# Performance work log

Measured on AMD Instinct MI355X. Metric: run time of the kernel, lower is better.

The kernel has to match this reference:

```python
import jax, jax.numpy as jnp
import numpy as np

ALPHA = 1.0
MIN_FEATURE_SIZE = 1.0
SC = 1e-12
EPS_V_FLOOR = 1e-32 ** (1.0 / 6.0)  # ~4.64e-6, floor on gradient magnitude


def setup_inputs() -> dict:
    key = jax.random.key(0)
    eps = jax.random.normal(key, (8192, 8192), dtype=jnp.float32)
    grid_size = jnp.asarray(0.05, dtype=jnp.float32)
    return {"eps": eps, "grid_size": grid_size}


def _ls_derivatives(phi, d):
    # torch.gradient == numpy.gradient with edge_order=1 (central interior, one-sided edges)
    phi_x, phi_y = jnp.gradient(phi, d, d)
    phi_x = phi_x + SC
    phi_y = phi_y + SC
    phi_xx, phi_xy = jnp.gradient(phi_x, d, d)        # second derivs of phi_x
    phi_yy = jnp.gradient(phi_y, d, axis=1)           # only d/dy of phi_y is used
    return phi_x, phi_y, phi_xx, phi_xy, phi_yy


def reference(eps, grid_size):
    ex, ey, exx, exy, eyy = _ls_derivatives(eps, grid_size)
    pi_d = jnp.pi / (1.1 * MIN_FEATURE_SIZE)
    eps_v = jnp.maximum(jnp.sqrt(ex * ex + ey * ey), jnp.float32(EPS_V_FLOOR))
    k = (ex * ex * eyy - 2.0 * ex * ey * exy + ey * ey * exx) / (eps_v ** 3)
    curve_const = jnp.abs(k * jnp.arctan(eps_v / (eps + 1e-6))) - pi_d
    return jnp.nansum(ALPHA * jnp.maximum(curve_const, 0.0) * grid_size ** 2)
```

## Files before the change

kernel.cpp:

```cpp
#include <hip/hip_runtime.h>
#include <math.h>


typedef float f2 __attribute__((ext_vector_type(2)));
typedef float f4 __attribute__((ext_vector_type(4), aligned(4)));

constexpr float SCF = 1e-12f;
constexpr float EVF = 4.6415888336e-6f;
constexpr float PID = 2.8559933214452666f;
constexpr float PIH = 1.5707963268f;
constexpr int   RS  = 64;

struct Row { f4 lo, hi; };

__device__ __forceinline__ float C(const Row& r, int k) {
    return k < 4 ? r.lo[k] : r.hi[k - 4];
}
__device__ __forceinline__ void load_row(Row& r, const float* p) {
    r.lo = *(const f4*)p;
    r.hi = *(const f4*)(p + 4);
}
__device__ __forceinline__ f2 mk(float a, float b) { f2 v; v.x = a; v.y = b; return v; }
__device__ __forceinline__ f2 fma2(f2 a, f2 b, f2 c) { return __builtin_elementwise_fma(a, b, c); }
__device__ __forceinline__ f2 max2(f2 a, f2 b) { return __builtin_elementwise_max(a, b); }
__device__ __forceinline__ f2 min2(f2 a, f2 b) { return __builtin_elementwise_min(a, b); }
__device__ __forceinline__ f2 abs2(f2 a) { return __builtin_elementwise_abs(a); }
__device__ __forceinline__ f2 rcp2(f2 a) {
    return mk(__builtin_amdgcn_rcpf(a.x), __builtin_amdgcn_rcpf(a.y));
}
__device__ __forceinline__ f2 sqrt2(f2 a) {
    return mk(__builtin_amdgcn_sqrtf(a.x), __builtin_amdgcn_sqrtf(a.y));
}

__device__ __forceinline__ f2 compute_pair(const Row& R0, const Row& R1,
                                           const Row& R2, const Row& R3,
                                           const Row& R4, const Row& R5,
                                           f2 inv2d, f2 inv4dd) {
    f2 dif[6];
    #pragma unroll
    for (int k = 0; k < 6; ++k)
        dif[k] = mk(C(R3, k + 1) - C(R1, k + 1),
                    C(R4, k + 1) - C(R2, k + 1));
    f2 Pz[8];
    #pragma unroll
    for (int k = 0; k < 8; ++k)
        Pz[k] = mk(C(R2, k), C(R3, k));

    const f2 sc2 = mk(SCF, SCF);
    f2 part = mk(0.0f, 0.0f);
    #pragma unroll
    for (int q = 0; q < 4; ++q) {
        const f2 c00 = Pz[q + 2];
        const f2 ex  = fma2(dif[q + 1], inv2d, sc2);
        const f2 ey  = fma2(Pz[q + 3] - Pz[q + 1], inv2d, sc2);
        const f2 sxx = mk(C(R4, q + 2) + C(R0, q + 2),
                          C(R5, q + 2) + C(R1, q + 2));
        const f2 exx = (sxx - 2.0f * c00) * inv4dd;
        const f2 eyy = (Pz[q + 4] + Pz[q] - 2.0f * c00) * inv4dd;
        const f2 exy = (dif[q + 2] - dif[q]) * inv4dd;

        const f2 ev  = max2(sqrt2(fma2(ex, ex, ey * ey)), mk(EVF, EVF));
        const f2 num = fma2(ex * ex, eyy,
                       fma2(-2.0f * (ex * ey), exy, (ey * ey) * exx));
        const f2 kabs = abs2(num) * rcp2(ev * ev * ev);

        const f2 aw = abs2(c00 + 1e-6f);
        const f2 mx = max2(ev, aw);
        const f2 mn = min2(ev, aw);
        const f2 t  = mn * rcp2(mx);
        const f2 t2 = t * t;
        f2 pl = fma2(t2, mk(-0.01172120f, -0.01172120f), mk(0.05265332f, 0.05265332f));
        pl = fma2(t2, pl, mk(-0.11643287f, -0.11643287f));
        pl = fma2(t2, pl, mk(0.19354346f, 0.19354346f));
        pl = fma2(t2, pl, mk(-0.33262347f, -0.33262347f));
        pl = fma2(t2, pl, mk(0.99997726f, 0.99997726f));
        pl = pl * t;
        f2 at;
        at.x = (ev.x > aw.x) ? PIH - pl.x : pl.x;
        at.y = (ev.y > aw.y) ? PIH - pl.y : pl.y;

        part = part + max2(fma2(kabs, at, mk(-PID, -PID)), mk(0.0f, 0.0f));
    }
    return part;
}

__device__ __forceinline__ float eg(const float* __restrict__ e, int n, int i, int j) {
    return e[(size_t)i * (size_t)n + j];
}
__device__ __forceinline__ float gex(const float* __restrict__ e, int n, int i, int j,
                                     float inv_d, float inv_2d) {
    float v;
    if (i == 0)          v = (eg(e, n, 1, j) - eg(e, n, 0, j)) * inv_d;
    else if (i == n - 1) v = (eg(e, n, n - 1, j) - eg(e, n, n - 2, j)) * inv_d;
    else                 v = (eg(e, n, i + 1, j) - eg(e, n, i - 1, j)) * inv_2d;
    return v + SCF;
}
__device__ __forceinline__ float gey(const float* __restrict__ e, int n, int i, int j,
                                     float inv_d, float inv_2d) {
    float v;
    if (j == 0)          v = (eg(e, n, i, 1) - eg(e, n, i, 0)) * inv_d;
    else if (j == n - 1) v = (eg(e, n, i, n - 1) - eg(e, n, i, n - 2)) * inv_d;
    else                 v = (eg(e, n, i, j + 1) - eg(e, n, i, j - 1)) * inv_2d;
    return v + SCF;
}

__global__ __launch_bounds__(256, 4)
void fab_fused(const float* __restrict__ eps, const float* __restrict__ gs,
               float* __restrict__ out, int n, int G, int nfr) {
    const float d       = *gs;
    const float inv_2d  = 0.5f / d;
    const float inv_4dd = inv_2d * inv_2d;

    float acc = 0.0f;

    if (threadIdx.x < 96) {
        const int bflat = blockIdx.y * gridDim.x + blockIdx.x;
        const int idx = bflat * 96 + (int)threadIdx.x;
        if (idx < nfr) {
            const float inv_d = inv_2d + inv_2d;
            int i, j;
            if (idx < 4 * n) {
                const int rr = (idx >= n) + (idx >= 2 * n) + (idx >= 3 * n);
                j = idx - rr * n;
                i = (rr < 2) ? rr : (n - 4) + rr;
            } else {
                const int t = idx - 4 * n;
                i = 2 + (t >> 3);
                const int cc = t & 7;
                j = (cc < 4) ? cc : (n - 8) + cc;
            }

            const float ex0 = gex(eps, n, i, j, inv_d, inv_2d);
            const float ey0 = gey(eps, n, i, j, inv_d, inv_2d);

            float exx, exy, eyy;
            if (i == 0)
                exx = (gex(eps, n, 1, j, inv_d, inv_2d) - ex0) * inv_d;
            else if (i == n - 1)
                exx = (ex0 - gex(eps, n, n - 2, j, inv_d, inv_2d)) * inv_d;
            else
                exx = (gex(eps, n, i + 1, j, inv_d, inv_2d)
                     - gex(eps, n, i - 1, j, inv_d, inv_2d)) * inv_2d;

            if (j == 0)
                exy = (gex(eps, n, i, 1, inv_d, inv_2d) - ex0) * inv_d;
            else if (j == n - 1)
                exy = (ex0 - gex(eps, n, i, n - 2, inv_d, inv_2d)) * inv_d;
            else
                exy = (gex(eps, n, i, j + 1, inv_d, inv_2d)
                     - gex(eps, n, i, j - 1, inv_d, inv_2d)) * inv_2d;

            if (j == 0)
                eyy = (gey(eps, n, i, 1, inv_d, inv_2d) - ey0) * inv_d;
            else if (j == n - 1)
                eyy = (ey0 - gey(eps, n, i, n - 2, inv_d, inv_2d)) * inv_d;
            else
                eyy = (gey(eps, n, i, j + 1, inv_d, inv_2d)
                     - gey(eps, n, i, j - 1, inv_d, inv_2d)) * inv_2d;

            const float ev = fmaxf(__builtin_amdgcn_sqrtf(fmaf(ex0, ex0, ey0 * ey0)), EVF);
            const float num = fmaf(ex0 * ex0, eyy,
                              fmaf(-2.0f * ex0 * ey0, exy, ey0 * ey0 * exx));
            const float kabs = fabsf(num) * __builtin_amdgcn_rcpf(ev * ev * ev);

            const float aw = fabsf(eg(eps, n, i, j) + 1e-6f);
            const float mx = fmaxf(ev, aw);
            const float mn = fminf(ev, aw);
            const float t  = mn * __builtin_amdgcn_rcpf(mx);
            const float t2 = t * t;
            float pl = fmaf(t2, -0.01172120f, 0.05265332f);
            pl = fmaf(t2, pl, -0.11643287f);
            pl = fmaf(t2, pl, 0.19354346f);
            pl = fmaf(t2, pl, -0.33262347f);
            pl = fmaf(t2, pl, 0.99997726f);
            pl *= t;
            const float at = (ev > aw) ? (PIH - pl) : pl;

            acc += fmaxf(fmaf(kabs, at, -PID), 0.0f);
        }
    }

    {
        const int gg = blockIdx.x * 256 + threadIdx.x;
        const bool valid = (gg >= 1) && (gg <= G);
        const int gc = min(max(gg, 1), G);
        const int j  = 4 * gc;
        const int i0 = 2 + RS * blockIdx.y;
        const int count = min(RS, (n - 2) - i0);
        const float*  pj = eps + (j - 2);
        const size_t  sn = (size_t)n;
        const f2 inv2d2  = mk(inv_2d, inv_2d);
        const f2 inv4dd2 = mk(inv_4dd, inv_4dd);

        Row s0, s1, s2, s3, s4, s5, s6, s7;
        load_row(s0, pj + (size_t)(i0 - 2) * sn);
        load_row(s1, pj + (size_t)(i0 - 1) * sn);
        load_row(s2, pj + (size_t)(i0    ) * sn);
        load_row(s3, pj + (size_t)(i0 + 1) * sn);
        load_row(s4, pj + (size_t)(i0 + 2) * sn);
        load_row(s5, pj + (size_t)(i0 + 3) * sn);
        const float* pnext = pj + (size_t)(i0 + 4) * sn;

        f2 acc2 = mk(0.0f, 0.0f);
        #define PHASEP(ph, A0, A1, A2, A3, A4, A5, L0, L1)                    \
        {                                                                     \
            const int k = kbase + 2 * (ph);                                   \
            if (k < count) {                                                  \
                if (k + 2 < count) {                                          \
                    load_row(L0, pnext);                                      \
                    load_row(L1, pnext + sn);                                 \
                }                                                             \
                pnext += 2 * sn;                                              \
                acc2 = acc2 + compute_pair(A0, A1, A2, A3, A4, A5,            \
                                           inv2d2, inv4dd2);                  \
            }                                                                 \
        }

        #pragma unroll 1
        for (int kbase = 0; kbase < RS; kbase += 8) {
            PHASEP(0, s0, s1, s2, s3, s4, s5, s6, s7)
            PHASEP(1, s2, s3, s4, s5, s6, s7, s0, s1)
            PHASEP(2, s4, s5, s6, s7, s0, s1, s2, s3)
            PHASEP(3, s6, s7, s0, s1, s2, s3, s4, s5)
        }
        #undef PHASEP

        if (valid) acc += acc2.x + acc2.y;
    }

    __shared__ float wsum[4];
    #pragma unroll
    for (int off = 32; off; off >>= 1)
        acc += __shfl_down(acc, off, 64);
    if ((threadIdx.x & 63) == 0) wsum[threadIdx.x >> 6] = acc;
    __syncthreads();
    if (threadIdx.x == 0)
        atomicAdd(out, (wsum[0] + wsum[1] + wsum[2] + wsum[3]) * d * d);
}

extern "C" void kernel_launch(void* const* d_in, const int* in_sizes, int n_in,
                              void* d_out, int out_size, void* d_ws, size_t ws_size,
                              hipStream_t stream) {
    const float* eps = (const float*)d_in[0];
    const float* gs  = (const float*)d_in[1];
    float* out = (float*)d_out;

    const long long tot = (long long)in_sizes[0];
    const int n = (int)(sqrt((double)tot) + 0.5);

    hipMemsetAsync(out, 0, sizeof(float), stream);

    const int G = (n - 8) / 4;
    const int nstrip = (n - 4 + RS - 1) / RS;
    const int nfr = 4 * n + 8 * (n - 4);

    dim3 block(256, 1);
    dim3 grid(n / 1024, nstrip);
    fab_fused<<<grid, block, 0, stream>>>(eps, gs, out, n, G, nfr);
}
```

Baseline: 92.13 us.

## Align stencil column windows for 16-byte loads, use rsqrt, slot-spread atomics

```diff
diff --git a/kernel.cpp b/kernel.cpp
--- a/kernel.cpp
+++ b/kernel.cpp
@@ -3,7 +3,7 @@
 
 
 typedef float f2 __attribute__((ext_vector_type(2)));
-typedef float f4 __attribute__((ext_vector_type(4), aligned(4)));
+typedef float f4 __attribute__((ext_vector_type(4)));
 
 constexpr float SCF = 1e-12f;
 constexpr float EVF = 4.6415888336e-6f;
@@ -28,8 +28,8 @@
 __device__ __forceinline__ f2 rcp2(f2 a) {
     return mk(__builtin_amdgcn_rcpf(a.x), __builtin_amdgcn_rcpf(a.y));
 }
-__device__ __forceinline__ f2 sqrt2(f2 a) {
-    return mk(__builtin_amdgcn_sqrtf(a.x), __builtin_amdgcn_sqrtf(a.y));
+__device__ __forceinline__ f2 rsq2(f2 a) {
+    return mk(__builtin_amdgcn_rsqf(a.x), __builtin_amdgcn_rsqf(a.y));
 }
 
 __device__ __forceinline__ f2 compute_pair(const Row& R0, const Row& R1,
@@ -59,10 +59,13 @@
         const f2 eyy = (Pz[q + 4] + Pz[q] - 2.0f * c00) * inv4dd;
         const f2 exy = (dif[q + 2] - dif[q]) * inv4dd;
 
-        const f2 ev  = max2(sqrt2(fma2(ex, ex, ey * ey)), mk(EVF, EVF));
+        const f2 s2  = fma2(ex, ex, ey * ey);
+        const f2 rsq = rsq2(s2);
+        const f2 ev  = max2(s2 * rsq, mk(EVF, EVF));
+        const f2 iv3 = min2(rsq * rsq * rsq, mk(1e16f, 1e16f));
         const f2 num = fma2(ex * ex, eyy,
                        fma2(-2.0f * (ex * ey), exy, (ey * ey) * exx));
-        const f2 kabs = abs2(num) * rcp2(ev * ev * ev);
+        const f2 kabs = abs2(num) * iv3;
 
         const f2 aw = abs2(c00 + 1e-6f);
         const f2 mx = max2(ev, aw);
@@ -106,7 +109,7 @@
 
 __global__ __launch_bounds__(256, 4)
 void fab_fused(const float* __restrict__ eps, const float* __restrict__ gs,
-               float* __restrict__ out, int n, int G, int nfr) {
+               float* __restrict__ ws, int n, int G2, int nfr) {
     const float d       = *gs;
     const float inv_2d  = 0.5f / d;
     const float inv_4dd = inv_2d * inv_2d;
@@ -127,7 +130,7 @@
                 const int t = idx - 4 * n;
                 i = 2 + (t >> 3);
                 const int cc = t & 7;
-                j = (cc < 4) ? cc : (n - 8) + cc;
+                j = (cc < 2) ? cc : (n - 8) + cc;
             }
 
             const float ex0 = gex(eps, n, i, j, inv_d, inv_2d);
@@ -182,12 +185,11 @@
 
     {
         const int gg = blockIdx.x * 256 + threadIdx.x;
-        const bool valid = (gg >= 1) && (gg <= G);
-        const int gc = min(max(gg, 1), G);
-        const int j  = 4 * gc;
+        const bool valid = gg < G2;
+        const int gc = min(gg, G2 - 1);
         const int i0 = 2 + RS * blockIdx.y;
         const int count = min(RS, (n - 2) - i0);
-        const float*  pj = eps + (j - 2);
+        const float*  pj = eps + 4 * (size_t)gc;
         const size_t  sn = (size_t)n;
         const f2 inv2d2  = mk(inv_2d, inv_2d);
         const f2 inv4dd2 = mk(inv_4dd, inv_4dd);
@@ -234,8 +236,21 @@
         acc += __shfl_down(acc, off, 64);
     if ((threadIdx.x & 63) == 0) wsum[threadIdx.x >> 6] = acc;
     __syncthreads();
-    if (threadIdx.x == 0)
-        atomicAdd(out, (wsum[0] + wsum[1] + wsum[2] + wsum[3]) * d * d);
+    if (threadIdx.x == 0) {
+        const int slot = (blockIdx.y * gridDim.x + blockIdx.x) & 63;
+        atomicAdd(&ws[slot], wsum[0] + wsum[1] + wsum[2] + wsum[3]);
+    }
+}
+
+__global__ __launch_bounds__(64)
+void fab_finish(const float* __restrict__ ws, const float* __restrict__ gs,
+                float* __restrict__ out) {
+    const float d = *gs;
+    float v = ws[threadIdx.x];
+    #pragma unroll
+    for (int off = 32; off; off >>= 1)
+        v += __shfl_down(v, off, 64);
+    if (threadIdx.x == 0) out[0] = v * d * d;
 }
 
 extern "C" void kernel_launch(void* const* d_in, const int* in_sizes, int n_in,
@@ -244,17 +259,19 @@
     const float* eps = (const float*)d_in[0];
     const float* gs  = (const float*)d_in[1];
     float* out = (float*)d_out;
+    float* ws  = (float*)d_ws;
 
     const long long tot = (long long)in_sizes[0];
     const int n = (int)(sqrt((double)tot) + 0.5);
 
-    hipMemsetAsync(out, 0, sizeof(float), stream);
-
-    const int G = (n - 8) / 4;
+    hipMemsetAsync(ws, 0, 64 * sizeof(float), stream);
+
+    const int G2  = (n - 8) / 4;
     const int nstrip = (n - 4 + RS - 1) / RS;
     const int nfr = 4 * n + 8 * (n - 4);
 
     dim3 block(256, 1);
     dim3 grid(n / 1024, nstrip);
-    fab_fused<<<grid, block, 0, stream>>>(eps, gs, out, n, G, nfr);
-}
+    fab_fused<<<grid, block, 0, stream>>>(eps, gs, ws, n, G2, nfr);
+    fab_finish<<<1, 64, 0, stream>>>(ws, gs, out);
+}
```

Result: slower. 94.46 us (+2.5%).
